# Kernel tuning notes

Measured on AMD Instinct MI355X. Metric: run time of the kernel, lower is better.

The kernel has to match this reference:

```python
import jax, jax.numpy as jnp
import numpy as np

HIDDEN = 1024
HEADS = 16
HEAD_DIM = HIDDEN // HEADS  # 64
B, S = 2, 2048


def setup_inputs() -> dict:
    key = jax.random.key(0)
    ks = jax.random.split(key, 12)
    lim_h = 1.0 / np.sqrt(HEAD_DIM)
    lim_o = 1.0 / np.sqrt(HIDDEN)
    u = lambda k, shape, lim: jax.random.uniform(k, shape, jnp.float32, -lim, lim)
    return {
        "query": jax.random.normal(ks[0], (B, S, HIDDEN), jnp.float32),
        "key": jax.random.normal(ks[1], (B, S, HIDDEN), jnp.float32),
        "value": jax.random.normal(ks[2], (B, S, HIDDEN), jnp.float32),
        "mask": jax.random.randint(ks[3], (B, 1, S, S), 0, 2, jnp.int32),
        "Wq": u(ks[4], (HEAD_DIM, HEAD_DIM), lim_h), "bq": u(ks[5], (HEAD_DIM,), lim_h),
        "Wk": u(ks[6], (HEAD_DIM, HEAD_DIM), lim_h), "bk": u(ks[7], (HEAD_DIM,), lim_h),
        "Wv": u(ks[8], (HEAD_DIM, HEAD_DIM), lim_h), "bv": u(ks[9], (HEAD_DIM,), lim_h),
        "Wo": u(ks[10], (HIDDEN, HIDDEN), lim_o), "bo": u(ks[11], (HIDDEN,), lim_o),
    }


def reference(query, key, value, mask, Wq, bq, Wk, bk, Wv, bv, Wo, bo):
    b = query.shape[0]
    # view [B, S, H, D]; per-head linear is SHARED across heads (head_dim x head_dim)
    q = query.reshape(b, -1, HEADS, HEAD_DIM) @ Wq.T + bq
    k = key.reshape(b, -1, HEADS, HEAD_DIM) @ Wk.T + bk
    v = value.reshape(b, -1, HEADS, HEAD_DIM) @ Wv.T + bv
    scores = jnp.einsum('nqhd,nkhd->nhqk', q, k)  # [B, H, Sq, Sk]
    scores = jnp.where(mask == 0, jnp.float32(-1e20), scores)
    # NOTE: original scales by sqrt(hidden_dim), not sqrt(head_dim)
    attn = jax.nn.softmax(scores / np.sqrt(HIDDEN).astype(np.float32), axis=3)
    out = jnp.einsum('nhql,nlhd->nqhd', attn, v).reshape(b, query.shape[1], HIDDEN)
    return out @ Wo.T + bo
```

## Files before the change

kernel.cpp:

```cpp
#include <hip/hip_runtime.h>
#include <hip/hip_bf16.h>

#define NB 2
#define NS 2048
#define NH 16
#define ND 64
#define NHID 1024

#define QSCALE 0.045084220f

typedef __attribute__((ext_vector_type(8))) short bf16x8;
typedef __attribute__((ext_vector_type(4))) short s16x4;
typedef __attribute__((ext_vector_type(4))) float f32x4;

typedef __attribute__((address_space(3))) unsigned int lds_u32;
typedef __attribute__((address_space(1))) unsigned int glb_u32;

__device__ inline void gl_lds16(const void* g, void* l) {
  __builtin_amdgcn_global_load_lds((const glb_u32*)g, (lds_u32*)l, 16, 0, 0);
}

__device__ inline short f2bf(float f) {
  __hip_bfloat16 h = __float2bfloat16(f);
  short s; __builtin_memcpy(&s, &h, 2); return s;
}

__device__ inline bf16x8 cvt8(const float* __restrict__ p) {
  float4 x = *(const float4*)p;
  float4 y = *(const float4*)(p + 4);
  bf16x8 r;
  r[0] = f2bf(x.x); r[1] = f2bf(x.y); r[2] = f2bf(x.z); r[3] = f2bf(x.w);
  r[4] = f2bf(y.x); r[5] = f2bf(y.y); r[6] = f2bf(y.z); r[7] = f2bf(y.w);
  return r;
}

__global__ __launch_bounds__(256) void prep(
    const int* __restrict__ mask, unsigned* __restrict__ mp,
    const float* __restrict__ Wq, const float* __restrict__ Wk,
    const float* __restrict__ Wv, const float* __restrict__ Wo,
    short* __restrict__ Wq_b, short* __restrict__ Wk_b,
    short* __restrict__ Wv_b, short* __restrict__ Wo_b)
{
  if (blockIdx.x < 1024) {
    int idx = blockIdx.x * 256 + threadIdx.x;
    const int4* src = (const int4*)(mask + (long)idx * 32);
    unsigned w = 0;
#pragma unroll
    for (int i = 0; i < 8; ++i) {
      int4 v = src[i];
      w |= (v.x != 0 ? 1u : 0u) << (i * 4 + 0);
      w |= (v.y != 0 ? 1u : 0u) << (i * 4 + 1);
      w |= (v.z != 0 ? 1u : 0u) << (i * 4 + 2);
      w |= (v.w != 0 ? 1u : 0u) << (i * 4 + 3);
    }
    mp[idx] = w;
  } else {
    int i = ((blockIdx.x - 1024) * 256 + threadIdx.x) * 4;
    const float* src; short* dst; int off; float sc = 1.0f;
    if (i < 1048576)      { src = Wo; dst = Wo_b; off = i; }
    else {
      int j = i - 1048576;
      if (j < 4096)       { src = Wq; dst = Wq_b; off = j; sc = QSCALE; }
      else if (j < 8192)  { src = Wk; dst = Wk_b; off = j - 4096; }
      else                { src = Wv; dst = Wv_b; off = j - 8192; }
    }
    float4 v = *(const float4*)(src + off);
    s16x4 o;
    o[0] = f2bf(v.x * sc); o[1] = f2bf(v.y * sc);
    o[2] = f2bf(v.z * sc); o[3] = f2bf(v.w * sc);
    *(s16x4*)(dst + off) = o;
  }
}

__global__ __launch_bounds__(256) void qk_proj(
    const float* __restrict__ qin, const float* __restrict__ kin,
    const short* __restrict__ Wq_b, const float* __restrict__ bq,
    const short* __restrict__ Wk_b, const float* __restrict__ bk,
    short* __restrict__ Qws, short* __restrict__ Kws)
{
  __shared__ __align__(16) short ldsT[4][16][72];
  const int tid = threadIdx.x;
  const int w = tid >> 6, lane = tid & 63;
  const int c = lane & 15, qq = lane >> 4;
  const int t = blockIdx.x * 4 + w;
  const int b = t >> 11, s = t & (NS - 1);
  const int aoff = (t * 16 + c) * 64 + qq * 8;
  const int row0 = lane >> 3, inner = lane & 7;

#pragma unroll
  for (int m = 0; m < 2; ++m) {
    const float* X  = (m == 0) ? qin  : kin;
    const short* W  = (m == 0) ? Wq_b : Wk_b;
    const float* bb = (m == 0) ? bq   : bk;
    short* dst      = (m == 0) ? Qws  : Kws;
    const float bsc = (m == 0) ? QSCALE : 1.0f;

    bf16x8 a0 = cvt8(X + aoff);
    bf16x8 a1 = cvt8(X + aoff + 32);

#pragma unroll
    for (int nt = 0; nt < 4; ++nt) {
      f32x4 z = {0.f, 0.f, 0.f, 0.f};
      const short* wp = W + (nt * 16 + c) * 64 + qq * 8;
      bf16x8 b0 = *(const bf16x8*)(wp);
      bf16x8 b1 = *(const bf16x8*)(wp + 32);
      z = __builtin_amdgcn_mfma_f32_16x16x32_bf16(a0, b0, z, 0, 0, 0);
      z = __builtin_amdgcn_mfma_f32_16x16x32_bf16(a1, b1, z, 0, 0, 0);
      float bias = bb[nt * 16 + c] * bsc;
#pragma unroll
      for (int r = 0; r < 4; ++r)
        ldsT[w][qq * 4 + r][nt * 16 + c] = f2bf(z[r] + bias);
    }

    bf16x8 v0 = *(const bf16x8*)&ldsT[w][row0][inner * 8];
    bf16x8 v1 = *(const bf16x8*)&ldsT[w][row0 + 8][inner * 8];
    int bh0 = b * NH + row0, bh1 = b * NH + row0 + 8;
    *(bf16x8*)(dst + (bh0 * NS + s) * 64 + inner * 8) = v0;
    *(bf16x8*)(dst + (bh1 * NS + s) * 64 + inner * 8) = v1;
  }
}

__global__ __launch_bounds__(256) void vproj(
    const float* __restrict__ vin, const short* __restrict__ Wv_b,
    const float* __restrict__ bv, short* __restrict__ Vt)
{
  __shared__ __align__(16) short ldsVT[64][72];
  const int tid = threadIdx.x;
  const int g = tid >> 6, lane = tid & 63;
  const int c = lane & 15, qq = lane >> 4;
  const int bh = blockIdx.x >> 5;
  const int stile = blockIdx.x & 31;
  const int b = bh >> 4, h = bh & 15;
  const int sb = stile * 64;

  bf16x8 wv[8];
  float bias[4];
#pragma unroll
  for (int nt = 0; nt < 4; ++nt) {
    const short* wp = Wv_b + (nt * 16 + c) * 64 + qq * 8;
    wv[nt * 2]     = *(const bf16x8*)(wp);
    wv[nt * 2 + 1] = *(const bf16x8*)(wp + 32);
    bias[nt] = bv[nt * 16 + c];
  }

  const float* ap = vin + ((size_t)((b * NS + sb + 16 * g + c) * 16 + h)) * 64 + qq * 8;
  bf16x8 a0 = cvt8(ap);
  bf16x8 a1 = cvt8(ap + 32);
#pragma unroll
  for (int nt = 0; nt < 4; ++nt) {
    f32x4 z = {0.f, 0.f, 0.f, 0.f};
    z = __builtin_amdgcn_mfma_f32_16x16x32_bf16(a0, wv[nt * 2], z, 0, 0, 0);
    z = __builtin_amdgcn_mfma_f32_16x16x32_bf16(a1, wv[nt * 2 + 1], z, 0, 0, 0);
    ushort4 u;
    u.x = (unsigned short)f2bf(z[0] + bias[nt]);
    u.y = (unsigned short)f2bf(z[1] + bias[nt]);
    u.z = (unsigned short)f2bf(z[2] + bias[nt]);
    u.w = (unsigned short)f2bf(z[3] + bias[nt]);
    *(ushort4*)&ldsVT[nt * 16 + c][16 * g + qq * 4] = u;
  }
  __syncthreads();

#pragma unroll
  for (int j = 0; j < 2; ++j) {
    int idx = tid + 256 * j;
    int d = idx >> 3, unit = idx & 7;
    bf16x8 o = *(const bf16x8*)&ldsVT[d][unit * 8];
    *(bf16x8*)(Vt + ((size_t)(bh * 64 + d)) * NS + sb + unit * 8) = o;
  }
}

__global__ __launch_bounds__(256) void attn(
    const short* __restrict__ Qws, const short* __restrict__ Kws,
    const short* __restrict__ Vt, const unsigned* __restrict__ Mp,
    short* __restrict__ AO)
{
  __shared__ __align__(16) short Ks[2][64][64];
  __shared__ __align__(16) short Vs[2][64][64];
  __shared__ __align__(16) short Ps[4][32][72];

  const int tid = threadIdx.x;
  const int w = tid >> 6, lane = tid & 63;
  const int c = lane & 15, qq = lane >> 4;
  const int bh = blockIdx.x & 31;
  const int qtile = blockIdx.x >> 5;
  const int b = bh >> 4, h = bh & 15;
  const int qbase = qtile * 128 + w * 32;

  const short* Qp = Qws + (size_t)bh * (NS * 64);
  const short* Kp = Kws + (size_t)bh * (NS * 64);
  const short* Vp = Vt + (size_t)bh * (64 * NS);
  const unsigned* mrow = Mp + (size_t)b * (NS * (NS / 32));

  bf16x8 aq[2][2];
#pragma unroll
  for (int nq = 0; nq < 2; ++nq) {
    const short* qp = Qp + (qbase + nq * 16 + c) * 64 + qq * 8;
    aq[nq][0] = *(const bf16x8*)(qp);
    aq[nq][1] = *(const bf16x8*)(qp + 32);
  }

  float lsum[2] = {0.f, 0.f};
  f32x4 O[2][4];
#pragma unroll
  for (int nq = 0; nq < 2; ++nq)
#pragma unroll
    for (int dt = 0; dt < 4; ++dt) { f32x4 z = {0.f, 0.f, 0.f, 0.f}; O[nq][dt] = z; }

  const int srow = lane >> 3;
  const int sunit = (lane & 7) ^ srow;
  auto stage = [&](int kt, int buf) {
#pragma unroll
    for (int i = 0; i < 2; ++i) {
      int j = w * 2 + i;
      const short* gk = Kp + ((size_t)(kt * 64 + j * 8 + srow)) * 64 + sunit * 8;
      gl_lds16(gk, &Ks[buf][0][0] + j * 512);
      const short* gv = Vp + ((size_t)(j * 8 + srow)) * NS + kt * 64 + sunit * 8;
      gl_lds16(gv, &Vs[buf][0][0] + j * 512);
    }
  };

  stage(0, 0);
  __syncthreads();

  for (int kt = 0; kt < NS / 64; ++kt) {
    const int buf = kt & 1;
    if (kt < NS / 64 - 1) stage(kt + 1, buf ^ 1);

    uint2 mw[2];
#pragma unroll
    for (int nq = 0; nq < 2; ++nq)
      mw[nq] = *(const uint2*)(mrow +
          (size_t)(qbase + nq * 16 + c) * (NS / 32) + kt * 2);

    f32x4 st[4][2];
#pragma unroll
    for (int mt = 0; mt < 4; ++mt) {
      const short* kb = &Ks[buf][mt * 16 + c][0];
      bf16x8 ak0 = *(const bf16x8*)(kb + ((qq ^ (c & 7)) << 3));
      bf16x8 ak1 = *(const bf16x8*)(kb + (((4 + qq) ^ (c & 7)) << 3));
#pragma unroll
      for (int nq = 0; nq < 2; ++nq) {
        f32x4 z = {0.f, 0.f, 0.f, 0.f};
        z = __builtin_amdgcn_mfma_f32_16x16x32_bf16(ak0, aq[nq][0], z, 0, 0, 0);
        z = __builtin_amdgcn_mfma_f32_16x16x32_bf16(ak1, aq[nq][1], z, 0, 0, 0);
        st[mt][nq] = z;
      }
    }

#pragma unroll
    for (int mt = 0; mt < 4; ++mt) {
#pragma unroll
      for (int nq = 0; nq < 2; ++nq) {
        unsigned wsel = (mt & 2) ? mw[nq].y : mw[nq].x;
        unsigned nib = (wsel >> (((mt & 1) << 4) + (qq << 2))) & 0xFu;
        f32x4 s = st[mt][nq];
        float e0 = (nib & 1u) ? __builtin_amdgcn_exp2f(s[0]) : 0.f;
        float e1 = (nib & 2u) ? __builtin_amdgcn_exp2f(s[1]) : 0.f;
        float e2 = (nib & 4u) ? __builtin_amdgcn_exp2f(s[2]) : 0.f;
        float e3 = (nib & 8u) ? __builtin_amdgcn_exp2f(s[3]) : 0.f;
        lsum[nq] += (e0 + e1) + (e2 + e3);
        ushort4 u;
        u.x = (unsigned short)f2bf(e0);
        u.y = (unsigned short)f2bf(e1);
        u.z = (unsigned short)f2bf(e2);
        u.w = (unsigned short)f2bf(e3);
        *(ushort4*)&Ps[w][nq * 16 + c][mt * 16 + (qq << 2)] = u;
      }
    }

#pragma unroll
    for (int ks = 0; ks < 2; ++ks) {
      bf16x8 pf[2];
#pragma unroll
      for (int nq = 0; nq < 2; ++nq)
        pf[nq] = *(const bf16x8*)&Ps[w][nq * 16 + c][ks * 32 + qq * 8];
#pragma unroll
      for (int dt = 0; dt < 4; ++dt) {
        const short* vb = &Vs[buf][dt * 16 + c][0];
        bf16x8 vf = *(const bf16x8*)(vb + ((((ks << 2) + qq) ^ (c & 7)) << 3));
#pragma unroll
        for (int nq = 0; nq < 2; ++nq)
          O[nq][dt] = __builtin_amdgcn_mfma_f32_16x16x32_bf16(vf, pf[nq], O[nq][dt], 0, 0, 0);
      }
    }

    __syncthreads();
  }

#pragma unroll
  for (int nq = 0; nq < 2; ++nq) {
    float v = lsum[nq];
    v += __shfl_xor(v, 16);
    v += __shfl_xor(v, 32);
    lsum[nq] = 1.0f / fmaxf(v, 1e-30f);
  }

#pragma unroll
  for (int nq = 0; nq < 2; ++nq) {
    int row = qbase + nq * 16 + c;
#pragma unroll
    for (int dt = 0; dt < 4; ++dt) {
      ushort4 u;
      u.x = (unsigned short)f2bf(O[nq][dt][0] * lsum[nq]);
      u.y = (unsigned short)f2bf(O[nq][dt][1] * lsum[nq]);
      u.z = (unsigned short)f2bf(O[nq][dt][2] * lsum[nq]);
      u.w = (unsigned short)f2bf(O[nq][dt][3] * lsum[nq]);
      *(ushort4*)(AO + ((size_t)(b * NS + row)) * NHID + h * 64 + dt * 16 + qq * 4) = u;
    }
  }
}

__global__ __launch_bounds__(256, 2) void oproj(
    const short* __restrict__ X, const short* __restrict__ Wo_b,
    const float* __restrict__ bo, float* __restrict__ out)
{
  __shared__ __align__(16) short As[2][64][64];
  __shared__ __align__(16) short Bs[2][128][64];
  const int tid = threadIdx.x;
  const int w = tid >> 6, lane = tid & 63;
  const int c = lane & 15, qq = lane >> 4;
  const int rowbase = blockIdx.x * 64;
  const int colbase = blockIdx.y * 128;
  const int mh = w & 1, nh = w >> 1;

  const int srow = lane >> 3;
  const int sunit = (lane & 7) ^ srow;

  auto stage = [&](int kb, int buf) {
#pragma unroll
    for (int i = 0; i < 6; ++i) {
      int t = w * 6 + i;
      if (t < 8) {
        const short* g = X + (size_t)(rowbase + t * 8 + srow) * NHID
                           + kb * 64 + sunit * 8;
        gl_lds16(g, &As[buf][0][0] + t * 512);
      } else {
        int j = t - 8;
        const short* g = Wo_b + (size_t)(colbase + j * 8 + srow) * NHID
                              + kb * 64 + sunit * 8;
        gl_lds16(g, &Bs[buf][0][0] + j * 512);
      }
    }
  };

  f32x4 acc[2][4];
#pragma unroll
  for (int mt = 0; mt < 2; ++mt)
#pragma unroll
    for (int nt = 0; nt < 4; ++nt) { f32x4 z = {0.f, 0.f, 0.f, 0.f}; acc[mt][nt] = z; }

  stage(0, 0);
  __syncthreads();

  for (int kb = 0; kb < NHID / 64; ++kb) {
    const int buf = kb & 1;
    if (kb < NHID / 64 - 1) stage(kb + 1, buf ^ 1);

    bf16x8 af[2][2];
#pragma unroll
    for (int mt = 0; mt < 2; ++mt) {
      const short* ap = &As[buf][mh * 32 + mt * 16 + c][0];
#pragma unroll
      for (int ks = 0; ks < 2; ++ks)
        af[mt][ks] = *(const bf16x8*)(ap + ((((ks << 2) + qq) ^ (c & 7)) << 3));
    }
#pragma unroll
    for (int nt = 0; nt < 4; ++nt) {
      const short* bp = &Bs[buf][nh * 64 + nt * 16 + c][0];
#pragma unroll
      for (int ks = 0; ks < 2; ++ks) {
        bf16x8 bf = *(const bf16x8*)(bp + ((((ks << 2) + qq) ^ (c & 7)) << 3));
#pragma unroll
        for (int mt = 0; mt < 2; ++mt)
          acc[mt][nt] = __builtin_amdgcn_mfma_f32_16x16x32_bf16(af[mt][ks], bf, acc[mt][nt], 0, 0, 0);
      }
    }

    __syncthreads();
  }

#pragma unroll
  for (int nt = 0; nt < 4; ++nt) {
    int col = colbase + nh * 64 + nt * 16 + c;
    float bias = bo[col];
#pragma unroll
    for (int mt = 0; mt < 2; ++mt) {
      int row = rowbase + mh * 32 + mt * 16 + qq * 4;
#pragma unroll
      for (int r = 0; r < 4; ++r)
        out[(size_t)(row + r) * NHID + col] = acc[mt][nt][r] + bias;
    }
  }
}

extern "C" void kernel_launch(void* const* d_in, const int* in_sizes, int n_in,
                              void* d_out, int out_size, void* d_ws, size_t ws_size,
                              hipStream_t stream) {
  const float* qin = (const float*)d_in[0];
  const float* kin = (const float*)d_in[1];
  const float* vin = (const float*)d_in[2];
  const int*  mask = (const int*)d_in[3];
  const float* Wq = (const float*)d_in[4];
  const float* bq = (const float*)d_in[5];
  const float* Wk = (const float*)d_in[6];
  const float* bk = (const float*)d_in[7];
  const float* Wv = (const float*)d_in[8];
  const float* bv = (const float*)d_in[9];
  const float* Wo = (const float*)d_in[10];
  const float* bo = (const float*)d_in[11];
  float* out = (float*)d_out;

  char* ws = (char*)d_ws;
  short* Qws = (short*)(ws);
  short* Kws = (short*)(ws + (size_t)(8 << 20));
  short* Vt  = (short*)(ws + (size_t)(16 << 20));
  short* AO  = (short*)(ws + (size_t)(24 << 20));
  unsigned* Mp = (unsigned*)(ws + (size_t)(32 << 20));
  short* Wo_b = (short*)(ws + (size_t)(33 << 20));
  short* Wq_b = (short*)(ws + (size_t)(35 << 20));
  short* Wk_b = (short*)(ws + (size_t)(35 << 20) + 8192);
  short* Wv_b = (short*)(ws + (size_t)(35 << 20) + 16384);

  prep<<<2060, 256, 0, stream>>>(mask, Mp, Wq, Wk, Wv, Wo, Wq_b, Wk_b, Wv_b, Wo_b);
  qk_proj<<<NB * NS / 4, 256, 0, stream>>>(qin, kin, Wq_b, bq, Wk_b, bk, Qws, Kws);
  vproj<<<(NB * NH) * (NS / 64), 256, 0, stream>>>(vin, Wv_b, bv, Vt);
  attn<<<(NB * NH) * (NS / 128), 256, 0, stream>>>(Qws, Kws, Vt, Mp, AO);
  oproj<<<dim3(64, 8), 256, 0, stream>>>(AO, Wo_b, bo, out);
}
```

Measured before the change: 224.5 us.

## Repack mask into wave-uniform 64-bit lane masks and halve attention query tile

The prep kernel now packs the mask into 64-bit words laid out per MFMA fragment, so each wave loads scalar lane masks and applies them with a single v_cndmask instead of per-lane bit extraction. The attention kernel drops from 32 to 16 query rows per wave (64 per block), doubling the grid and adding an occupancy hint of 4 blocks per CU. The P staging buffer is shrunk and XOR-swizzled to avoid LDS bank conflicts. The smaller tile halves K/V reuse per block, which doubles K/V global and LDS traffic in exchange for lower register pressure and more parallelism. The mask data is also read as 16 scalar loads per iteration.

```diff
diff --git a/kernel.cpp b/kernel.cpp
--- a/kernel.cpp
+++ b/kernel.cpp
@@ -23,6 +23,12 @@
 __device__ inline short f2bf(float f) {
   __hip_bfloat16 h = __float2bfloat16(f);
   short s; __builtin_memcpy(&s, &h, 2); return s;
+}
+
+__device__ inline float selbit(float e, unsigned long long m) {
+  float r;
+  asm("v_cndmask_b32 %0, 0, %1, %2" : "=v"(r) : "v"(e), "s"(m));
+  return r;
 }
 
 __device__ inline bf16x8 cvt8(const float* __restrict__ p) {
@@ -35,27 +41,41 @@
 }
 
 __global__ __launch_bounds__(256) void prep(
-    const int* __restrict__ mask, unsigned* __restrict__ mp,
+    const int* __restrict__ mask, unsigned long long* __restrict__ mp,
     const float* __restrict__ Wq, const float* __restrict__ Wk,
     const float* __restrict__ Wv, const float* __restrict__ Wo,
     short* __restrict__ Wq_b, short* __restrict__ Wk_b,
     short* __restrict__ Wv_b, short* __restrict__ Wo_b)
 {
-  if (blockIdx.x < 1024) {
-    int idx = blockIdx.x * 256 + threadIdx.x;
-    const int4* src = (const int4*)(mask + (long)idx * 32);
-    unsigned w = 0;
-#pragma unroll
-    for (int i = 0; i < 8; ++i) {
-      int4 v = src[i];
-      w |= (v.x != 0 ? 1u : 0u) << (i * 4 + 0);
-      w |= (v.y != 0 ? 1u : 0u) << (i * 4 + 1);
-      w |= (v.z != 0 ? 1u : 0u) << (i * 4 + 2);
-      w |= (v.w != 0 ? 1u : 0u) << (i * 4 + 3);
-    }
-    mp[idx] = w;
+  if (blockIdx.x < 512) {
+    int tg = blockIdx.x * 256 + threadIdx.x;
+    int q4 = tg & 3;
+    int g4 = tg >> 2;
+    int mt = g4 & 3, kt = (g4 >> 2) & 31, qg = (g4 >> 7) & 127, b = g4 >> 14;
+    unsigned long long wq[4] = {0ull, 0ull, 0ull, 0ull};
+#pragma unroll
+    for (int cc = 0; cc < 4; ++cc) {
+      int c2 = q4 * 4 + cc;
+      const int4* p = (const int4*)(mask +
+          ((size_t)(b * NS + qg * 16 + c2) * NS) + kt * 64 + mt * 16);
+#pragma unroll
+      for (int qq2 = 0; qq2 < 4; ++qq2) {
+        int4 v = p[qq2];
+        int sh = qq2 * 16 + c2;
+        wq[0] |= (unsigned long long)(v.x != 0) << sh;
+        wq[1] |= (unsigned long long)(v.y != 0) << sh;
+        wq[2] |= (unsigned long long)(v.z != 0) << sh;
+        wq[3] |= (unsigned long long)(v.w != 0) << sh;
+      }
+    }
+#pragma unroll
+    for (int r = 0; r < 4; ++r) {
+      wq[r] |= __shfl_xor(wq[r], 1);
+      wq[r] |= __shfl_xor(wq[r], 2);
+    }
+    mp[(size_t)g4 * 4 + q4] = wq[q4];
   } else {
-    int i = ((blockIdx.x - 1024) * 256 + threadIdx.x) * 4;
+    int i = ((blockIdx.x - 512) * 256 + threadIdx.x) * 4;
     const float* src; short* dst; int off; float sc = 1.0f;
     if (i < 1048576)      { src = Wo; dst = Wo_b; off = i; }
     else {
@@ -169,14 +189,14 @@
   }
 }
 
-__global__ __launch_bounds__(256) void attn(
+__global__ __launch_bounds__(256, 4) void attn(
     const short* __restrict__ Qws, const short* __restrict__ Kws,
-    const short* __restrict__ Vt, const unsigned* __restrict__ Mp,
+    const short* __restrict__ Vt, const unsigned long long* __restrict__ Mp,
     short* __restrict__ AO)
 {
   __shared__ __align__(16) short Ks[2][64][64];
   __shared__ __align__(16) short Vs[2][64][64];
-  __shared__ __align__(16) short Ps[4][32][72];
+  __shared__ __align__(16) short Ps[4][16][64];
 
   const int tid = threadIdx.x;
   const int w = tid >> 6, lane = tid & 63;
@@ -184,27 +204,30 @@
   const int bh = blockIdx.x & 31;
   const int qtile = blockIdx.x >> 5;
   const int b = bh >> 4, h = bh & 15;
-  const int qbase = qtile * 128 + w * 32;
+  const int qbase = qtile * 64 + w * 16;
+  const int ca2 = (lane & 7) << 1;
 
   const short* Qp = Qws + (size_t)bh * (NS * 64);
   const short* Kp = Kws + (size_t)bh * (NS * 64);
   const short* Vp = Vt + (size_t)bh * (64 * NS);
-  const unsigned* mrow = Mp + (size_t)b * (NS * (NS / 32));
-
-  bf16x8 aq[2][2];
-#pragma unroll
-  for (int nq = 0; nq < 2; ++nq) {
-    const short* qp = Qp + (qbase + nq * 16 + c) * 64 + qq * 8;
-    aq[nq][0] = *(const bf16x8*)(qp);
-    aq[nq][1] = *(const bf16x8*)(qp + 32);
-  }
-
-  float lsum[2] = {0.f, 0.f};
-  f32x4 O[2][4];
-#pragma unroll
-  for (int nq = 0; nq < 2; ++nq)
-#pragma unroll
-    for (int dt = 0; dt < 4; ++dt) { f32x4 z = {0.f, 0.f, 0.f, 0.f}; O[nq][dt] = z; }
+
+  const int wu = __builtin_amdgcn_readfirstlane(w);
+  const unsigned long long* mbase =
+      Mp + (size_t)(b * (NS / 16) + qtile * 4 + wu) * ((NS / 64) * 16);
+
+  bf16x8 aq0, aq1;
+  {
+    const short* qp = Qp + (qbase + c) * 64 + qq * 8;
+    aq0 = *(const bf16x8*)(qp);
+    aq1 = *(const bf16x8*)(qp + 32);
+  }
+
+  float lsum = 0.f;
+  f32x4 O[4];
+#pragma unroll
+  for (int dt = 0; dt < 4; ++dt) { f32x4 z = {0.f, 0.f, 0.f, 0.f}; O[dt] = z; }
+
+  short* Pw = &Ps[w][c][0];
 
   const int srow = lane >> 3;
   const int sunit = (lane & 7) ^ srow;
@@ -226,87 +249,68 @@
     const int buf = kt & 1;
     if (kt < NS / 64 - 1) stage(kt + 1, buf ^ 1);
 
-    uint2 mw[2];
-#pragma unroll
-    for (int nq = 0; nq < 2; ++nq)
-      mw[nq] = *(const uint2*)(mrow +
-          (size_t)(qbase + nq * 16 + c) * (NS / 32) + kt * 2);
-
-    f32x4 st[4][2];
+    unsigned long long mw[16];
+#pragma unroll
+    for (int i = 0; i < 16; ++i) mw[i] = mbase[(size_t)kt * 16 + i];
+
+    f32x4 st[4];
 #pragma unroll
     for (int mt = 0; mt < 4; ++mt) {
       const short* kb = &Ks[buf][mt * 16 + c][0];
       bf16x8 ak0 = *(const bf16x8*)(kb + ((qq ^ (c & 7)) << 3));
       bf16x8 ak1 = *(const bf16x8*)(kb + (((4 + qq) ^ (c & 7)) << 3));
-#pragma unroll
-      for (int nq = 0; nq < 2; ++nq) {
-        f32x4 z = {0.f, 0.f, 0.f, 0.f};
-        z = __builtin_amdgcn_mfma_f32_16x16x32_bf16(ak0, aq[nq][0], z, 0, 0, 0);
-        z = __builtin_amdgcn_mfma_f32_16x16x32_bf16(ak1, aq[nq][1], z, 0, 0, 0);
-        st[mt][nq] = z;
-      }
+      f32x4 z = {0.f, 0.f, 0.f, 0.f};
+      z = __builtin_amdgcn_mfma_f32_16x16x32_bf16(ak0, aq0, z, 0, 0, 0);
+      z = __builtin_amdgcn_mfma_f32_16x16x32_bf16(ak1, aq1, z, 0, 0, 0);
+      st[mt] = z;
     }
 
 #pragma unroll
     for (int mt = 0; mt < 4; ++mt) {
-#pragma unroll
-      for (int nq = 0; nq < 2; ++nq) {
-        unsigned wsel = (mt & 2) ? mw[nq].y : mw[nq].x;
-        unsigned nib = (wsel >> (((mt & 1) << 4) + (qq << 2))) & 0xFu;
-        f32x4 s = st[mt][nq];
-        float e0 = (nib & 1u) ? __builtin_amdgcn_exp2f(s[0]) : 0.f;
-        float e1 = (nib & 2u) ? __builtin_amdgcn_exp2f(s[1]) : 0.f;
-        float e2 = (nib & 4u) ? __builtin_amdgcn_exp2f(s[2]) : 0.f;
-        float e3 = (nib & 8u) ? __builtin_amdgcn_exp2f(s[3]) : 0.f;
-        lsum[nq] += (e0 + e1) + (e2 + e3);
-        ushort4 u;
-        u.x = (unsigned short)f2bf(e0);
-        u.y = (unsigned short)f2bf(e1);
-        u.z = (unsigned short)f2bf(e2);
-        u.w = (unsigned short)f2bf(e3);
-        *(ushort4*)&Ps[w][nq * 16 + c][mt * 16 + (qq << 2)] = u;
-      }
+      f32x4 s = st[mt];
+      float e0 = selbit(__builtin_amdgcn_exp2f(s[0]), mw[mt * 4 + 0]);
+      float e1 = selbit(__builtin_amdgcn_exp2f(s[1]), mw[mt * 4 + 1]);
+      float e2 = selbit(__builtin_amdgcn_exp2f(s[2]), mw[mt * 4 + 2]);
+      float e3 = selbit(__builtin_amdgcn_exp2f(s[3]), mw[mt * 4 + 3]);
+      lsum += (e0 + e1) + (e2 + e3);
+      ushort4 u;
+      u.x = (unsigned short)f2bf(e0);
+      u.y = (unsigned short)f2bf(e1);
+      u.z = (unsigned short)f2bf(e2);
+      u.w = (unsigned short)f2bf(e3);
+      *(ushort4*)&Pw[((mt * 4 + qq) ^ ca2) << 2] = u;
     }
 
 #pragma unroll
     for (int ks = 0; ks < 2; ++ks) {
-      bf16x8 pf[2];
-#pragma unroll
-      for (int nq = 0; nq < 2; ++nq)
-        pf[nq] = *(const bf16x8*)&Ps[w][nq * 16 + c][ks * 32 + qq * 8];
+      bf16x8 pf = *(const bf16x8*)&Pw[((ks * 8 + qq * 2) ^ ca2) << 2];
 #pragma unroll
       for (int dt = 0; dt < 4; ++dt) {
         const short* vb = &Vs[buf][dt * 16 + c][0];
         bf16x8 vf = *(const bf16x8*)(vb + ((((ks << 2) + qq) ^ (c & 7)) << 3));
-#pragma unroll
-        for (int nq = 0; nq < 2; ++nq)
-          O[nq][dt] = __builtin_amdgcn_mfma_f32_16x16x32_bf16(vf, pf[nq], O[nq][dt], 0, 0, 0);
+        O[dt] = __builtin_amdgcn_mfma_f32_16x16x32_bf16(vf, pf, O[dt], 0, 0, 0);
       }
     }
 
     __syncthreads();
   }
 
-#pragma unroll
-  for (int nq = 0; nq < 2; ++nq) {
-    float v = lsum[nq];
+  {
+    float v = lsum;
     v += __shfl_xor(v, 16);
     v += __shfl_xor(v, 32);
-    lsum[nq] = 1.0f / fmaxf(v, 1e-30f);
-  }
-
-#pragma unroll
-  for (int nq = 0; nq < 2; ++nq) {
-    int row = qbase + nq * 16 + c;
-#pragma unroll
-    for (int dt = 0; dt < 4; ++dt) {
-      ushort4 u;
-      u.x = (unsigned short)f2bf(O[nq][dt][0] * lsum[nq]);
-      u.y = (unsigned short)f2bf(O[nq][dt][1] * lsum[nq]);
-      u.z = (unsigned short)f2bf(O[nq][dt][2] * lsum[nq]);
-      u.w = (unsigned short)f2bf(O[nq][dt][3] * lsum[nq]);
-      *(ushort4*)(AO + ((size_t)(b * NS + row)) * NHID + h * 64 + dt * 16 + qq * 4) = u;
-    }
+    lsum = 1.0f / fmaxf(v, 1e-30f);
+  }
+
+  const int row = qbase + c;
+#pragma unroll
+  for (int dt = 0; dt < 4; ++dt) {
+    ushort4 u;
+    u.x = (unsigned short)f2bf(O[dt][0] * lsum);
+    u.y = (unsigned short)f2bf(O[dt][1] * lsum);
+    u.z = (unsigned short)f2bf(O[dt][2] * lsum);
+    u.w = (unsigned short)f2bf(O[dt][3] * lsum);
+    *(ushort4*)(AO + ((size_t)(b * NS + row)) * NHID + h * 64 + dt * 16 + qq * 4) = u;
   }
 }
 
@@ -415,15 +419,15 @@
   short* Kws = (short*)(ws + (size_t)(8 << 20));
   short* Vt  = (short*)(ws + (size_t)(16 << 20));
   short* AO  = (short*)(ws + (size_t)(24 << 20));
-  unsigned* Mp = (unsigned*)(ws + (size_t)(32 << 20));
+  unsigned long long* Mp = (unsigned long long*)(ws + (size_t)(32 << 20));
   short* Wo_b = (short*)(ws + (size_t)(33 << 20));
   short* Wq_b = (short*)(ws + (size_t)(35 << 20));
   short* Wk_b = (short*)(ws + (size_t)(35 << 20) + 8192);
   short* Wv_b = (short*)(ws + (size_t)(35 << 20) + 16384);
 
-  prep<<<2060, 256, 0, stream>>>(mask, Mp, Wq, Wk, Wv, Wo, Wq_b, Wk_b, Wv_b, Wo_b);
+  prep<<<1548, 256, 0, stream>>>(mask, Mp, Wq, Wk, Wv, Wo, Wq_b, Wk_b, Wv_b, Wo_b);
   qk_proj<<<NB * NS / 4, 256, 0, stream>>>(qin, kin, Wq_b, bq, Wk_b, bk, Qws, Kws);
   vproj<<<(NB * NH) * (NS / 64), 256, 0, stream>>>(vin, Wv_b, bv, Vt);
-  attn<<<(NB * NH) * (NS / 128), 256, 0, stream>>>(Qws, Kws, Vt, Mp, AO);
+  attn<<<(NB * NH) * (NS / 64), 256, 0, stream>>>(Qws, Kws, Vt, Mp, AO);
   oproj<<<dim3(64, 8), 256, 0, stream>>>(AO, Wo_b, bo, out);
 }
```

After: 212.5 us. 1.06x faster.
